# Kernel tuning notes

Measured on AMD Instinct MI355X. Metric: run time of the kernel, lower is better.

Reference implementation:

```python
import jax, jax.numpy as jnp
import numpy as np

N, K, D = 100000, 16, 64


def setup_inputs() -> dict:
    key = jax.random.key(0)
    ks = jax.random.split(key, 7)
    coords = jax.random.normal(ks[0], (N, 3), dtype=jnp.float32)
    features = jax.random.normal(ks[1], (N, D), dtype=jnp.float32)
    W1 = jax.random.normal(ks[2], (10, D // 2), dtype=jnp.float32) * 0.3
    b1 = jax.random.normal(ks[3], (D // 2,), dtype=jnp.float32) * 0.1
    W2 = jax.random.normal(ks[4], (D // 2, D), dtype=jnp.float32) * 0.2
    b2 = jax.random.normal(ks[5], (D,), dtype=jnp.float32) * 0.1
    neighbor_idx = jax.random.randint(ks[6], (N, K), 0, N, dtype=jnp.int64)
    return {"coords": coords, "features": features, "W1": W1, "b1": b1,
            "W2": W2, "b2": b2, "neighbor_idx": neighbor_idx}


def reference(coords, features, W1, b1, W2, b2, neighbor_idx):
    n, k = neighbor_idx.shape
    d = features.shape[-1]
    # original_idx repeats each point K times -> broadcast along K
    original = jnp.broadcast_to(coords[:, None, :], (n, k, 3))
    neighbor = coords[neighbor_idx]                      # (N,K,3) gather
    relative = original - neighbor                       # (N,K,3)
    distance = jnp.linalg.norm(relative, axis=-1, keepdims=True)  # (N,K,1)
    concat = jnp.concatenate([original, neighbor, relative, distance], axis=-1)  # (N,K,10)
    h = jax.nn.relu(jnp.einsum('nkc,ch->nkh', concat, W1) + b1)   # (N,K,d/2)
    enc = jnp.einsum('nkh,hd->nkd', h, W2) + b2                   # (N,K,d)
    feat = jnp.broadcast_to(features[:, None, :], (n, k, d))      # features[original_idx]
    return jnp.concatenate([enc, feat], axis=-1)                  # (N,K,2d)
```

## Files before the change

kernel.cpp:

```cpp
#include <hip/hip_runtime.h>
#include <math.h>


#define HID 32
#define DF  64
#define RS  68

typedef float f4 __attribute__((ext_vector_type(4)));

__global__ __launch_bounds__(256) void lse_kernel(
    const float* __restrict__ coords,
    const float* __restrict__ features,
    const float* __restrict__ W1,
    const float* __restrict__ b1,
    const float* __restrict__ W2,
    const float* __restrict__ b2,
    const int*   __restrict__ nidx,
    float* __restrict__ out,
    long long total, int K, int kshift)
{
    __shared__ float smem[4][64][RS];

    const int t  = threadIdx.x;
    const int wv = t >> 6;
    const int l  = t & 63;
    const long long pbase = (long long)blockIdx.x * 256 + (long long)wv * 64;
    const long long p = pbase + l;

    if (p < total) {
        const int n = (kshift >= 0) ? (int)(p >> kshift) : (int)(p / K);
        const int j = nidx[p];

        const float ox = coords[3 * n + 0];
        const float oy = coords[3 * n + 1];
        const float oz = coords[3 * n + 2];
        const float nx = coords[3 * j + 0];
        const float ny = coords[3 * j + 1];
        const float nz = coords[3 * j + 2];
        const float rx = ox - nx, ry = oy - ny, rz = oz - nz;
        const float dist = sqrtf(rx * rx + ry * ry + rz * rz);
        const float c[10] = {ox, oy, oz, nx, ny, nz, rx, ry, rz, dist};

        float h[HID];
#pragma unroll
        for (int jj = 0; jj < HID; ++jj) {
            float acc = b1[jj];
#pragma unroll
            for (int cc = 0; cc < 10; ++cc) acc = fmaf(c[cc], W1[cc * HID + jj], acc);
            h[jj] = fmaxf(acc, 0.0f);
        }

        for (int c0 = 0; c0 < DF; c0 += 4) {
            float a0 = b2[c0 + 0], a1 = b2[c0 + 1], a2 = b2[c0 + 2], a3 = b2[c0 + 3];
#pragma unroll
            for (int jj = 0; jj < HID; ++jj) {
                const float hv = h[jj];
                const float* w = W2 + jj * DF + c0;
                a0 = fmaf(hv, w[0], a0);
                a1 = fmaf(hv, w[1], a1);
                a2 = fmaf(hv, w[2], a2);
                a3 = fmaf(hv, w[3], a3);
            }
            f4 v = {a0, a1, a2, a3};
            *reinterpret_cast<f4*>(&smem[wv][l][c0]) = v;
        }
    }

    __syncthreads();

    const int g = l >> 4;
    const int q = l & 15;
#pragma unroll 4
    for (int i = 0; i < 16; ++i) {
        const int r = 4 * i + g;
        const long long pr = pbase + r;
        if (pr < total) {
            float* orow = out + pr * (2 * DF);
            const f4 enc = *reinterpret_cast<const f4*>(&smem[wv][r][4 * q]);
            __builtin_nontemporal_store(enc, reinterpret_cast<f4*>(orow + 4 * q));
            const int nr = (kshift >= 0) ? (int)(pr >> kshift) : (int)(pr / K);
            const f4 f = *reinterpret_cast<const f4*>(features + (long long)nr * DF + 4 * q);
            __builtin_nontemporal_store(f, reinterpret_cast<f4*>(orow + DF + 4 * q));
        }
    }
}

extern "C" void kernel_launch(void* const* d_in, const int* in_sizes, int n_in,
                              void* d_out, int out_size, void* d_ws, size_t ws_size,
                              hipStream_t stream) {
    const float* coords   = (const float*)d_in[0];
    const float* features = (const float*)d_in[1];
    const float* W1       = (const float*)d_in[2];
    const float* b1       = (const float*)d_in[3];
    const float* W2       = (const float*)d_in[4];
    const float* b2       = (const float*)d_in[5];
    const int*   nidx     = (const int*)d_in[6];

    const int N = in_sizes[0] / 3;
    const int K = in_sizes[6] / N;
    const long long total = (long long)N * K;
    const int kshift = ((K & (K - 1)) == 0) ? __builtin_ctz(K) : -1;

    float* out = (float*)d_out;

    const int block = 256;
    const long long grid = (total + 255) / 256;
    lse_kernel<<<(unsigned)grid, block, 0, stream>>>(
        coords, features, W1, b1, W2, b2, nidx, out, total, K, kshift);
}
```

Baseline: 175.3 us.

## Stage MLP weights in LDS and split encoding transpose into two half-width passes

Each block now copies W1, b1, W2 and b2 into shared memory once and computes both MLP layers with float4 vector FMAs from LDS, instead of scalar global loads. The per-wave transpose tile is halved to 32 columns (RS 36), and the 64 encoder outputs are written in two passes that rely on wave-local waitcnt and sched barriers rather than a block-wide __syncthreads. The features copy is moved to its own loop. This lowers LDS use to raise occupancy and removes the global weight traffic, at the cost of an extra block-wide sync at entry and depending on wave-synchronous LDS ordering being correct.

```diff
diff --git a/kernel.cpp b/kernel.cpp
--- a/kernel.cpp
+++ b/kernel.cpp
@@ -4,7 +4,7 @@
 
 #define HID 32
 #define DF  64
-#define RS  68
+#define RS  36
 
 typedef float f4 __attribute__((ext_vector_type(4)));
 
@@ -19,68 +19,100 @@
     float* __restrict__ out,
     long long total, int K, int kshift)
 {
-    __shared__ float smem[4][64][RS];
+    __shared__ alignas(16) float sW1[10 * HID];
+    __shared__ alignas(16) float sb1[HID];
+    __shared__ alignas(16) float sW2[HID * DF];
+    __shared__ alignas(16) float sb2[DF];
+    __shared__ alignas(16) float tile[4][64][RS];
 
-    const int t  = threadIdx.x;
+    const int t = threadIdx.x;
+    {
+        f4* sW2v = (f4*)sW2;
+        const f4* W2v = (const f4*)W2;
+        for (int i = t; i < HID * DF / 4; i += 256) sW2v[i] = W2v[i];
+        if (t < 80) ((f4*)sW1)[t] = ((const f4*)W1)[t];
+        if (t >= 128 && t < 136) ((f4*)sb1)[t - 128] = ((const f4*)b1)[t - 128];
+        if (t >= 160 && t < 176) ((f4*)sb2)[t - 160] = ((const f4*)b2)[t - 160];
+    }
+    __syncthreads();
+
     const int wv = t >> 6;
     const int l  = t & 63;
     const long long pbase = (long long)blockIdx.x * 256 + (long long)wv * 64;
     const long long p = pbase + l;
+    const bool valid = p < total;
 
-    if (p < total) {
+    float h[HID];
+    if (valid) {
         const int n = (kshift >= 0) ? (int)(p >> kshift) : (int)(p / K);
         const int j = nidx[p];
-
-        const float ox = coords[3 * n + 0];
-        const float oy = coords[3 * n + 1];
-        const float oz = coords[3 * n + 2];
-        const float nx = coords[3 * j + 0];
-        const float ny = coords[3 * j + 1];
-        const float nz = coords[3 * j + 2];
+        const float ox = coords[3 * n + 0], oy = coords[3 * n + 1], oz = coords[3 * n + 2];
+        const float nx = coords[3 * j + 0], ny = coords[3 * j + 1], nz = coords[3 * j + 2];
         const float rx = ox - nx, ry = oy - ny, rz = oz - nz;
         const float dist = sqrtf(rx * rx + ry * ry + rz * rz);
         const float c[10] = {ox, oy, oz, nx, ny, nz, rx, ry, rz, dist};
 
-        float h[HID];
 #pragma unroll
-        for (int jj = 0; jj < HID; ++jj) {
-            float acc = b1[jj];
+        for (int j0 = 0; j0 < HID; j0 += 4) {
+            f4 acc = *(const f4*)&sb1[j0];
 #pragma unroll
-            for (int cc = 0; cc < 10; ++cc) acc = fmaf(c[cc], W1[cc * HID + jj], acc);
-            h[jj] = fmaxf(acc, 0.0f);
-        }
-
-        for (int c0 = 0; c0 < DF; c0 += 4) {
-            float a0 = b2[c0 + 0], a1 = b2[c0 + 1], a2 = b2[c0 + 2], a3 = b2[c0 + 3];
-#pragma unroll
-            for (int jj = 0; jj < HID; ++jj) {
-                const float hv = h[jj];
-                const float* w = W2 + jj * DF + c0;
-                a0 = fmaf(hv, w[0], a0);
-                a1 = fmaf(hv, w[1], a1);
-                a2 = fmaf(hv, w[2], a2);
-                a3 = fmaf(hv, w[3], a3);
+            for (int cc = 0; cc < 10; ++cc) {
+                const f4 w = *(const f4*)&sW1[cc * HID + j0];
+                acc += c[cc] * w;
             }
-            f4 v = {a0, a1, a2, a3};
-            *reinterpret_cast<f4*>(&smem[wv][l][c0]) = v;
+            h[j0 + 0] = fmaxf(acc[0], 0.0f);
+            h[j0 + 1] = fmaxf(acc[1], 0.0f);
+            h[j0 + 2] = fmaxf(acc[2], 0.0f);
+            h[j0 + 3] = fmaxf(acc[3], 0.0f);
         }
     }
 
-    __syncthreads();
+    const int q = l & 7;
+    const int g = l >> 3;
+#pragma unroll
+    for (int pass = 0; pass < 2; ++pass) {
+        if (valid) {
+#pragma unroll
+            for (int cg = 0; cg < 32; cg += 4) {
+                const int col = pass * 32 + cg;
+                f4 acc = *(const f4*)&sb2[col];
+#pragma unroll
+                for (int jj = 0; jj < HID; ++jj) {
+                    const f4 w = *(const f4*)&sW2[jj * DF + col];
+                    acc += h[jj] * w;
+                }
+                *(f4*)&tile[wv][l][cg] = acc;
+            }
+        }
+        asm volatile("s_waitcnt lgkmcnt(0)" ::: "memory");
+        __builtin_amdgcn_sched_barrier(0);
 
-    const int g = l >> 4;
-    const int q = l & 15;
+#pragma unroll
+        for (int i = 0; i < 8; ++i) {
+            const int r = 8 * i + g;
+            const long long pr = pbase + r;
+            if (pr < total) {
+                const f4 enc = *(const f4*)&tile[wv][r][4 * q];
+                __builtin_nontemporal_store(
+                    enc, (f4*)(out + pr * (2 * DF) + pass * 32 + 4 * q));
+            }
+        }
+        if (pass == 0) {
+            asm volatile("s_waitcnt lgkmcnt(0)" ::: "memory");
+            __builtin_amdgcn_sched_barrier(0);
+        }
+    }
+
+    const int q16 = l & 15;
+    const int g4  = l >> 4;
 #pragma unroll 4
     for (int i = 0; i < 16; ++i) {
-        const int r = 4 * i + g;
+        const int r = 4 * i + g4;
         const long long pr = pbase + r;
         if (pr < total) {
-            float* orow = out + pr * (2 * DF);
-            const f4 enc = *reinterpret_cast<const f4*>(&smem[wv][r][4 * q]);
-            __builtin_nontemporal_store(enc, reinterpret_cast<f4*>(orow + 4 * q));
             const int nr = (kshift >= 0) ? (int)(pr >> kshift) : (int)(pr / K);
-            const f4 f = *reinterpret_cast<const f4*>(features + (long long)nr * DF + 4 * q);
-            __builtin_nontemporal_store(f, reinterpret_cast<f4*>(orow + DF + 4 * q));
+            const f4 f = *(const f4*)(features + (long long)nr * DF + 4 * q16);
+            __builtin_nontemporal_store(f, (f4*)(out + pr * (2 * DF) + DF + 4 * q16));
         }
     }
 }
```

Measured after the change: 264.6 us. 1.51x slower.
